# Performance work log

Measured on AMD Instinct MI355X. Metric: run time of the kernel, lower is better.

Reference implementation:

```python
import jax, jax.numpy as jnp
import numpy as np

N_NODES = 100000
N_EDGES = 1600000
D = 128


def setup_inputs() -> dict:
    key = jax.random.key(0)
    ks = jax.random.split(key, 10)
    s = 1.0 / np.sqrt(D)
    return {
        "feat": jax.random.normal(ks[0], (N_NODES, D), dtype=jnp.float32),
        "W_self0": jax.random.normal(ks[1], (D, D), dtype=jnp.float32) * s,
        "W_neigh0": jax.random.normal(ks[2], (D, D), dtype=jnp.float32) * s,
        "b0": jnp.zeros((D,), dtype=jnp.float32),
        "W_self1": jax.random.normal(ks[3], (D, D), dtype=jnp.float32) * s,
        "W_neigh1": jax.random.normal(ks[4], (D, D), dtype=jnp.float32) * s,
        "b1": jnp.zeros((D,), dtype=jnp.float32),
        "ln_g": jnp.ones((D,), dtype=jnp.float32),
        "ln_b": jnp.zeros((D,), dtype=jnp.float32),
        "edge_src": jax.random.randint(ks[5], (N_EDGES,), 0, N_NODES, dtype=jnp.int32),
        "edge_dst": jax.random.randint(ks[6], (N_EDGES,), 0, N_NODES, dtype=jnp.int32),
        "in_deg": jax.random.randint(ks[7], (N_NODES,), 1, 64, dtype=jnp.int32),
    }


def _sage_layer(h, src, dst, inv_deg, W_self, W_neigh, b):
    # mean aggregation over incoming neighbors: gather -> segment_sum -> scale
    msg = jax.ops.segment_sum(h[src], dst, num_segments=N_NODES)  # [N, d]
    h_neigh = msg * inv_deg[:, None]
    return h @ W_self + h_neigh @ W_neigh + b


def _layer_norm(x, g, b, eps=1e-5):
    mu = jnp.mean(x, axis=-1, keepdims=True)
    var = jnp.mean((x - mu) ** 2, axis=-1, keepdims=True)
    return (x - mu) * jax.lax.rsqrt(var + eps) * g + b


def reference(feat, W_self0, W_neigh0, b0, W_self1, W_neigh1, b1, ln_g, ln_b,
              edge_src, edge_dst, in_deg):
    # Eval mode: dropout = identity, no EmbeddingSelector / reg loss.
    inv_deg = 1.0 / jnp.maximum(in_deg, 1).astype(feat.dtype)
    h = _sage_layer(feat, edge_src, edge_dst, inv_deg, W_self0, W_neigh0, b0)
    h = _layer_norm(h, ln_g, ln_b)
    h = jax.nn.relu(h)
    h = _sage_layer(h, edge_src, edge_dst, inv_deg, W_self1, W_neigh1, b1)
    return h
```

## Files before the change

### kernel.cpp

```cpp
#include <hip/hip_runtime.h>

#define D 128
#define NN 100000

typedef __attribute__((ext_vector_type(8))) short short8;
typedef __attribute__((ext_vector_type(16))) float floatx16;
typedef __attribute__((ext_vector_type(2))) float floatx2;

__device__ inline unsigned short bf16_rne(float f) {
    unsigned int u = __float_as_uint(f);
    u += 0x7fff + ((u >> 16) & 1);
    return (unsigned short)(u >> 16);
}
__device__ inline unsigned char fp8_enc1(float f) {
    return (unsigned char)(__builtin_amdgcn_cvt_pk_fp8_f32(f, f, 0, false) & 0xff);
}

__global__ __launch_bounds__(256) void prep_kernel(
    const float* __restrict__ feat, unsigned short* __restrict__ feat16,
    unsigned char* __restrict__ feat8,
    const float* __restrict__ Ws0, const float* __restrict__ Wn0,
    const float* __restrict__ Ws1, const float* __restrict__ Wn1,
    unsigned short* __restrict__ wt0, unsigned short* __restrict__ wt1,
    int* __restrict__ counts)
{
    int bid = blockIdx.x;
    if (bid < 12500) {
        int i = bid * 256 + threadIdx.x;
        float4 v = *(const float4*)(feat + (size_t)i * 4);
        unsigned short u[4] = { bf16_rne(v.x), bf16_rne(v.y), bf16_rne(v.z), bf16_rne(v.w) };
        *(uint2*)(feat16 + (size_t)i * 4) = *(uint2*)u;
        int w = __builtin_amdgcn_cvt_pk_fp8_f32(v.x, v.y, 0, false);
        w = __builtin_amdgcn_cvt_pk_fp8_f32(v.z, v.w, w, true);
        ((unsigned int*)feat8)[i] = (unsigned int)w;
    } else if (bid < 12756) {
        int i = (bid - 12500) * 256 + threadIdx.x;
        int layer = i >> 15;
        int r = i & 32767;
        int n = r >> 8;
        int k = r & 255;
        const float* Ws = layer ? Ws1 : Ws0;
        const float* Wn = layer ? Wn1 : Wn0;
        float v = (k < 128) ? Ws[(size_t)k * 128 + n] : Wn[(size_t)(k - 128) * 128 + n];
        unsigned short* wt = layer ? wt1 : wt0;
        wt[(size_t)n * 256 + k] = bf16_rne(v);
    } else {
        int i = (bid - 12756) * 256 + threadIdx.x;
        if (i < NN / 4) ((uint4*)counts)[i] = make_uint4(0u, 0u, 0u, 0u);
    }
}

__global__ __launch_bounds__(256) void hist_rank_kernel(
    const int* __restrict__ dst, int* __restrict__ counts,
    int* __restrict__ rank, int E)
{
    int e = blockIdx.x * 256 + threadIdx.x;
    if (e < E) rank[e] = atomicAdd(&counts[dst[e]], 1);
}

__global__ __launch_bounds__(256) void scan1_kernel(
    const int* __restrict__ counts, int* __restrict__ row_ptr,
    int* __restrict__ blockSums, int N)
{
    __shared__ int sd[256];
    int t = threadIdx.x;
    int base = blockIdx.x * 1024;
    int v[4]; int tot = 0;
#pragma unroll
    for (int i = 0; i < 4; i++) {
        int idx = base + t * 4 + i;
        v[i] = (idx < N) ? counts[idx] : 0;
        tot += v[i];
    }
    sd[t] = tot; __syncthreads();
    for (int off = 1; off < 256; off <<= 1) {
        int x = (t >= off) ? sd[t - off] : 0;
        __syncthreads();
        sd[t] += x;
        __syncthreads();
    }
    int excl = sd[t] - tot;
    if (t == 255) blockSums[blockIdx.x] = sd[255];
    int run = excl;
#pragma unroll
    for (int i = 0; i < 4; i++) {
        int idx = base + t * 4 + i;
        if (idx < N) row_ptr[idx] = run;
        run += v[i];
    }
}

__global__ __launch_bounds__(256) void scan2_kernel(
    const int* __restrict__ blockSums, int* __restrict__ blockOffs, int nb)
{
    __shared__ int sd[256];
    int t = threadIdx.x;
    int val = (t < nb) ? blockSums[t] : 0;
    sd[t] = val; __syncthreads();
    for (int off = 1; off < 256; off <<= 1) {
        int x = (t >= off) ? sd[t - off] : 0;
        __syncthreads();
        sd[t] += x;
        __syncthreads();
    }
    if (t < nb) blockOffs[t] = sd[t] - val;
}

__global__ __launch_bounds__(256) void scan3_kernel(
    int* __restrict__ row_ptr, const int* __restrict__ blockOffs, int N, int E)
{
    int i = blockIdx.x * 256 + threadIdx.x;
    if (i < N) row_ptr[i] += blockOffs[i >> 10];
    if (i == N) row_ptr[N] = E;
}

__global__ __launch_bounds__(256) void fill_stream_kernel(
    const int* __restrict__ src, const int* __restrict__ dst,
    const int* __restrict__ row_ptr, const int* __restrict__ rank,
    int* __restrict__ col, int E)
{
    int e = blockIdx.x * 256 + threadIdx.x;
    if (e >= E) return;
    col[row_ptr[dst[e]] + rank[e]] = src[e];
}

__global__ __launch_bounds__(256) void gather8_kernel(
    const unsigned char* __restrict__ h8, const int* __restrict__ row_ptr,
    const int* __restrict__ col, const int* __restrict__ in_deg,
    unsigned short* __restrict__ msg16, int N)
{
    const int wave = threadIdx.x >> 6;
    const int lane = threadIdx.x & 63;
    const int quad = lane >> 4;
    const int ln16 = lane & 15;
    const int node = (blockIdx.x * 4 + wave) * 4 + quad;
    if (node >= N) return;

    const size_t lo = (size_t)ln16 * 8;
    int beg = row_ptr[node];
    int end = row_ptr[node + 1];

    float f[8] = {0.f,0.f,0.f,0.f,0.f,0.f,0.f,0.f};
    int j = beg;
    for (; j + 4 <= end; j += 4) {
        int c0 = col[j], c1 = col[j + 1], c2 = col[j + 2], c3 = col[j + 3];
        uint2 u0 = *(const uint2*)(h8 + (size_t)c0 * D + lo);
        uint2 u1 = *(const uint2*)(h8 + (size_t)c1 * D + lo);
        uint2 u2 = *(const uint2*)(h8 + (size_t)c2 * D + lo);
        uint2 u3 = *(const uint2*)(h8 + (size_t)c3 * D + lo);
#pragma unroll
        for (int q = 0; q < 4; q++) {
            uint2 u = q == 0 ? u0 : q == 1 ? u1 : q == 2 ? u2 : u3;
            floatx2 p0 = __builtin_amdgcn_cvt_pk_f32_fp8((int)u.x, false);
            floatx2 p1 = __builtin_amdgcn_cvt_pk_f32_fp8((int)u.x, true);
            floatx2 p2 = __builtin_amdgcn_cvt_pk_f32_fp8((int)u.y, false);
            floatx2 p3 = __builtin_amdgcn_cvt_pk_f32_fp8((int)u.y, true);
            f[0] += p0.x; f[1] += p0.y; f[2] += p1.x; f[3] += p1.y;
            f[4] += p2.x; f[5] += p2.y; f[6] += p3.x; f[7] += p3.y;
        }
    }
    for (; j < end; ++j) {
        uint2 u = *(const uint2*)(h8 + (size_t)col[j] * D + lo);
        floatx2 p0 = __builtin_amdgcn_cvt_pk_f32_fp8((int)u.x, false);
        floatx2 p1 = __builtin_amdgcn_cvt_pk_f32_fp8((int)u.x, true);
        floatx2 p2 = __builtin_amdgcn_cvt_pk_f32_fp8((int)u.y, false);
        floatx2 p3 = __builtin_amdgcn_cvt_pk_f32_fp8((int)u.y, true);
        f[0] += p0.x; f[1] += p0.y; f[2] += p1.x; f[3] += p1.y;
        f[4] += p2.x; f[5] += p2.y; f[6] += p3.x; f[7] += p3.y;
    }
    int dg = in_deg[node];
    float invd = 1.f / (float)(dg > 1 ? dg : 1);
    unsigned short us[8];
#pragma unroll
    for (int i = 0; i < 8; i++) us[i] = bf16_rne(f[i] * invd);
    *(uint4*)(msg16 + (size_t)node * D + ln16 * 8) = *(const uint4*)us;
}

__global__ __launch_bounds__(256) void mfma32_kernel(
    const unsigned short* __restrict__ A16, const unsigned short* __restrict__ Msg16,
    const unsigned short* __restrict__ Wt,
    const float* __restrict__ bias,
    const float* __restrict__ ln_g, const float* __restrict__ ln_b,
    unsigned short* __restrict__ Out16, unsigned char* __restrict__ Out8,
    float* __restrict__ Out32, int N, int do_ln)
{
    __shared__ unsigned short sB[32768];

    const int tid  = threadIdx.x;
    const int wave = tid >> 6;
    const int lane = tid & 63;
    const int half = lane >> 5;
    const int n32  = lane & 31;
    const int wrow0 = blockIdx.x * 128 + wave * 32;

#pragma unroll
    for (int i = 0; i < 16; i++) {
        int idx = tid + i * 256;
        int n = idx & 127;
        int c = idx >> 7;
        uint4 w = *(const uint4*)(Wt + (size_t)n * 256 + c * 8);
        int hs = c >> 4, kc = (c >> 1) & 7, hf = c & 1;
        int ct = n >> 5, nn = n & 31;
        int chunk = (((ct * 2 + hs) * 8 + kc) * 2 + hf) * 32 + nn;
        *(uint4*)&sB[(size_t)chunk * 8] = w;
    }
    __syncthreads();

    const int arow = wrow0 + n32;
    const bool arv = arow < N;
    const size_t koff = (size_t)half * 8;

    floatx16 acc[4];
#pragma unroll
    for (int ct = 0; ct < 4; ct++)
#pragma unroll
        for (int r = 0; r < 16; r++) acc[ct][r] = 0.f;

#pragma unroll
    for (int hs = 0; hs < 2; hs++) {
        const unsigned short* Asrc = hs ? Msg16 : A16;
#pragma unroll
        for (int kc = 0; kc < 8; kc++) {
            short8 a;
            if (arv) a = *(const short8*)(Asrc + (size_t)arow * D + kc * 16 + koff);
            else     a = (short8){0,0,0,0,0,0,0,0};
#pragma unroll
            for (int ct = 0; ct < 4; ct++) {
                short8 b = *(const short8*)&sB[((size_t)((ct * 2 + hs) * 8 + kc) * 64 + lane) * 8];
                acc[ct] = __builtin_amdgcn_mfma_f32_32x32x16_bf16(a, b, acc[ct], 0, 0, 0);
            }
        }
    }

    float bb[4];
#pragma unroll
    for (int ct = 0; ct < 4; ct++) bb[ct] = bias[ct * 32 + n32];

    float v[4][16];
#pragma unroll
    for (int ct = 0; ct < 4; ct++)
#pragma unroll
        for (int r = 0; r < 16; r++) v[ct][r] = acc[ct][r] + bb[ct];

    if (do_ln) {
        float gg[4], be[4];
#pragma unroll
        for (int ct = 0; ct < 4; ct++) {
            gg[ct] = ln_g[ct * 32 + n32];
            be[ct] = ln_b[ct * 32 + n32];
        }
        float s[16], s2[16];
#pragma unroll
        for (int r = 0; r < 16; r++) {
            s[r]  = v[0][r] + v[1][r] + v[2][r] + v[3][r];
            s2[r] = v[0][r]*v[0][r] + v[1][r]*v[1][r] + v[2][r]*v[2][r] + v[3][r]*v[3][r];
        }
#pragma unroll
        for (int off = 1; off < 32; off <<= 1) {
#pragma unroll
            for (int r = 0; r < 16; r++) {
                s[r]  += __shfl_xor(s[r],  off);
                s2[r] += __shfl_xor(s2[r], off);
            }
        }
#pragma unroll
        for (int r = 0; r < 16; r++) {
            float mean = s[r] * (1.f / 128.f);
            float var  = s2[r] * (1.f / 128.f) - mean * mean;
            float rstd = rsqrtf(var + 1e-5f);
            int row_g = wrow0 + (r & 3) + 8 * (r >> 2) + 4 * half;
            if (row_g < N) {
#pragma unroll
                for (int ct = 0; ct < 4; ct++) {
                    float t = (v[ct][r] - mean) * rstd * gg[ct] + be[ct];
                    t = t > 0.f ? t : 0.f;
                    Out16[(size_t)row_g * D + ct * 32 + n32] = bf16_rne(t);
                    Out8[(size_t)row_g * D + ct * 32 + n32] = fp8_enc1(t);
                }
            }
        }
    } else {
#pragma unroll
        for (int r = 0; r < 16; r++) {
            int row_g = wrow0 + (r & 3) + 8 * (r >> 2) + 4 * half;
            if (row_g < N) {
#pragma unroll
                for (int ct = 0; ct < 4; ct++)
                    Out32[(size_t)row_g * D + ct * 32 + n32] = v[ct][r];
            }
        }
    }
}

extern "C" void kernel_launch(void* const* d_in, const int* in_sizes, int n_in,
                              void* d_out, int out_size, void* d_ws, size_t ws_size,
                              hipStream_t stream)
{
    const float* feat = (const float*)d_in[0];
    const float* Ws0  = (const float*)d_in[1];
    const float* Wn0  = (const float*)d_in[2];
    const float* b0   = (const float*)d_in[3];
    const float* Ws1  = (const float*)d_in[4];
    const float* Wn1  = (const float*)d_in[5];
    const float* b1   = (const float*)d_in[6];
    const float* lng  = (const float*)d_in[7];
    const float* lnb  = (const float*)d_in[8];
    const int* esrc   = (const int*)d_in[9];
    const int* edst   = (const int*)d_in[10];
    const int* indeg  = (const int*)d_in[11];

    const int N = NN;
    const int E = in_sizes[9];

    float* out = (float*)d_out;

    char* ws = (char*)d_ws;
    size_t o = 0;
    auto alloc = [&](size_t bytes) { char* p = ws + o; o += (bytes + 15) & ~(size_t)15; return p; };
    unsigned short* feat16 = (unsigned short*)alloc((size_t)N * D * 2);
    int* col     = (int*)alloc((size_t)E * 4);
    int* row_ptr = (int*)alloc((size_t)(N + 1) * 4);
    unsigned short* wt0 = (unsigned short*)alloc(128 * 256 * 2);
    unsigned short* wt1 = (unsigned short*)alloc(128 * 256 * 2);
    int* bsums = (int*)alloc(1024);
    int* boffs = (int*)alloc(1024);
    char* regD = alloc((size_t)N * D * 2 > ((size_t)N * 4 + (size_t)E * 4 + 32)
                       ? (size_t)N * D * 2 : ((size_t)N * 4 + (size_t)E * 4 + 32));
    int* counts = (int*)regD;
    int* rank   = (int*)(regD + (((size_t)N * 4 + 15) & ~(size_t)15));
    unsigned short* h116 = (unsigned short*)regD;

    unsigned short* msg0 = (unsigned short*)d_out;
    unsigned char*  feat8 = (unsigned char*)d_out + (size_t)N * D * 2;
    unsigned char*  h18   = (unsigned char*)d_out + (size_t)N * D * 3;
    unsigned short* msg1 = feat16;
    (void)ws_size;

    const int edge_blocks = (E + 255) / 256;
    const int gemm_blocks = (N + 127) / 128;
    const int gather_blocks = (N + 15) / 16;
    const int nb = (N + 1023) / 1024;
    const int zero_blocks = (N / 4 + 255) / 256;

    prep_kernel<<<12500 + 256 + zero_blocks, 256, 0, stream>>>(
        feat, feat16, feat8, Ws0, Wn0, Ws1, Wn1, wt0, wt1, counts);

    hist_rank_kernel<<<edge_blocks, 256, 0, stream>>>(edst, counts, rank, E);
    scan1_kernel<<<nb, 256, 0, stream>>>(counts, row_ptr, bsums, N);
    scan2_kernel<<<1, 256, 0, stream>>>(bsums, boffs, nb);
    scan3_kernel<<<(N + 256) / 256, 256, 0, stream>>>(row_ptr, boffs, N, E);
    fill_stream_kernel<<<edge_blocks, 256, 0, stream>>>(esrc, edst, row_ptr, rank, col, E);

    gather8_kernel<<<gather_blocks, 256, 0, stream>>>(feat8, row_ptr, col, indeg, msg0, N);
    mfma32_kernel<<<gemm_blocks, 256, 0, stream>>>(
        feat16, msg0, wt0, b0, lng, lnb, h116, h18, nullptr, N, 1);

    gather8_kernel<<<gather_blocks, 256, 0, stream>>>(h18, row_ptr, col, indeg, msg1, N);
    mfma32_kernel<<<gemm_blocks, 256, 0, stream>>>(
        h116, msg1, wt1, b1, nullptr, nullptr, nullptr, nullptr, out, N, 0);
}
```

Measured before the change: 371.8 us.

## Build CSR via two-level bucket partition instead of global atomic histogram

Replaces the global-atomic histogram, three-kernel scan and random scatter with a two-pass radix-style partition. Edges are first bucketed by dst>>8 using LDS histograms and packed src/low-dst pairs, then each bucket is sorted locally in LDS to produce row_ptr and col. The aim is to cut global atomic contention and scattered writes, giving more localized memory traffic. In exchange it adds a packed intermediate array and assumes src fits in 24 bits and N fits within 391*256 buckets.

```diff
diff --git a/kernel.cpp b/kernel.cpp
--- a/kernel.cpp
+++ b/kernel.cpp
@@ -2,6 +2,8 @@
 
 #define D 128
 #define NN 100000
+#define PB 391
+#define EPB 4096
 
 typedef __attribute__((ext_vector_type(8))) short short8;
 typedef __attribute__((ext_vector_type(16))) float floatx16;
@@ -21,8 +23,7 @@
     unsigned char* __restrict__ feat8,
     const float* __restrict__ Ws0, const float* __restrict__ Wn0,
     const float* __restrict__ Ws1, const float* __restrict__ Wn1,
-    unsigned short* __restrict__ wt0, unsigned short* __restrict__ wt1,
-    int* __restrict__ counts)
+    unsigned short* __restrict__ wt0, unsigned short* __restrict__ wt1)
 {
     int bid = blockIdx.x;
     if (bid < 12500) {
@@ -33,7 +34,7 @@
         int w = __builtin_amdgcn_cvt_pk_fp8_f32(v.x, v.y, 0, false);
         w = __builtin_amdgcn_cvt_pk_fp8_f32(v.z, v.w, w, true);
         ((unsigned int*)feat8)[i] = (unsigned int)w;
-    } else if (bid < 12756) {
+    } else {
         int i = (bid - 12500) * 256 + threadIdx.x;
         int layer = i >> 15;
         int r = i & 32767;
@@ -44,84 +45,108 @@
         float v = (k < 128) ? Ws[(size_t)k * 128 + n] : Wn[(size_t)(k - 128) * 128 + n];
         unsigned short* wt = layer ? wt1 : wt0;
         wt[(size_t)n * 256 + k] = bf16_rne(v);
-    } else {
-        int i = (bid - 12756) * 256 + threadIdx.x;
-        if (i < NN / 4) ((uint4*)counts)[i] = make_uint4(0u, 0u, 0u, 0u);
-    }
-}
-
-__global__ __launch_bounds__(256) void hist_rank_kernel(
-    const int* __restrict__ dst, int* __restrict__ counts,
-    int* __restrict__ rank, int E)
-{
-    int e = blockIdx.x * 256 + threadIdx.x;
-    if (e < E) rank[e] = atomicAdd(&counts[dst[e]], 1);
-}
-
-__global__ __launch_bounds__(256) void scan1_kernel(
-    const int* __restrict__ counts, int* __restrict__ row_ptr,
-    int* __restrict__ blockSums, int N)
-{
-    __shared__ int sd[256];
+    }
+}
+
+__global__ __launch_bounds__(256) void part_count_kernel(
+    const int* __restrict__ dst, unsigned int* __restrict__ bucketCnt,
+    unsigned int* __restrict__ blockBase, int E)
+{
+    __shared__ unsigned int h[PB];
+    const int t = threadIdx.x;
+    const int b = blockIdx.x;
+    for (int i = t; i < PB; i += 256) h[i] = 0;
+    __syncthreads();
+    const int base = b * EPB;
+#pragma unroll
+    for (int k = 0; k < EPB / 256; k++) {
+        int e = base + k * 256 + t;
+        if (e < E) atomicAdd(&h[(unsigned)dst[e] >> 8], 1u);
+    }
+    __syncthreads();
+    for (int i = t; i < PB; i += 256) {
+        unsigned int c = h[i];
+        unsigned int o = 0;
+        if (c) o = atomicAdd(&bucketCnt[i], c);
+        blockBase[(size_t)b * PB + i] = o;
+    }
+}
+
+__global__ __launch_bounds__(512) void part_scan_kernel(
+    const unsigned int* __restrict__ bucketCnt, unsigned int* __restrict__ bucketStart,
+    int E)
+{
+    __shared__ unsigned int sd[512];
     int t = threadIdx.x;
-    int base = blockIdx.x * 1024;
-    int v[4]; int tot = 0;
-#pragma unroll
-    for (int i = 0; i < 4; i++) {
-        int idx = base + t * 4 + i;
-        v[i] = (idx < N) ? counts[idx] : 0;
-        tot += v[i];
-    }
-    sd[t] = tot; __syncthreads();
-    for (int off = 1; off < 256; off <<= 1) {
-        int x = (t >= off) ? sd[t - off] : 0;
+    unsigned int v = (t < PB) ? bucketCnt[t] : 0u;
+    sd[t] = v; __syncthreads();
+    for (int off = 1; off < 512; off <<= 1) {
+        unsigned int x = (t >= off) ? sd[t - off] : 0u;
         __syncthreads();
         sd[t] += x;
         __syncthreads();
     }
-    int excl = sd[t] - tot;
-    if (t == 255) blockSums[blockIdx.x] = sd[255];
-    int run = excl;
-#pragma unroll
-    for (int i = 0; i < 4; i++) {
-        int idx = base + t * 4 + i;
-        if (idx < N) row_ptr[idx] = run;
-        run += v[i];
-    }
-}
-
-__global__ __launch_bounds__(256) void scan2_kernel(
-    const int* __restrict__ blockSums, int* __restrict__ blockOffs, int nb)
-{
-    __shared__ int sd[256];
-    int t = threadIdx.x;
-    int val = (t < nb) ? blockSums[t] : 0;
-    sd[t] = val; __syncthreads();
+    if (t < PB) bucketStart[t] = sd[t] - v;
+    if (t == 0) bucketStart[PB] = (unsigned int)E;
+}
+
+__global__ __launch_bounds__(256) void part_scatter_kernel(
+    const int* __restrict__ src, const int* __restrict__ dst,
+    const unsigned int* __restrict__ bucketStart,
+    const unsigned int* __restrict__ blockBase,
+    unsigned int* __restrict__ pairs, int E)
+{
+    __shared__ unsigned int h[PB];
+    const int t = threadIdx.x;
+    const int b = blockIdx.x;
+    for (int i = t; i < PB; i += 256) h[i] = 0;
+    __syncthreads();
+    const int base = b * EPB;
+#pragma unroll
+    for (int k = 0; k < EPB / 256; k++) {
+        int e = base + k * 256 + t;
+        if (e < E) {
+            unsigned int d = (unsigned int)dst[e];
+            unsigned int bk = d >> 8;
+            unsigned int lr = atomicAdd(&h[bk], 1u);
+            unsigned int pos = bucketStart[bk] + blockBase[(size_t)b * PB + bk] + lr;
+            pairs[pos] = ((unsigned int)src[e] << 8) | (d & 255u);
+        }
+    }
+}
+
+__global__ __launch_bounds__(256) void part_fine_kernel(
+    const unsigned int* __restrict__ pairs, const unsigned int* __restrict__ bucketStart,
+    int* __restrict__ row_ptr, int* __restrict__ col, int N, int E)
+{
+    __shared__ unsigned int h[256], sc[256], pos[256];
+    const int t = threadIdx.x;
+    const int b = blockIdx.x;
+    h[t] = 0;
+    __syncthreads();
+    const unsigned int ebeg = bucketStart[b];
+    const unsigned int eend = bucketStart[b + 1];
+    for (unsigned int i = ebeg + t; i < eend; i += 256)
+        atomicAdd(&h[pairs[i] & 255u], 1u);
+    __syncthreads();
+    sc[t] = h[t]; __syncthreads();
     for (int off = 1; off < 256; off <<= 1) {
-        int x = (t >= off) ? sd[t - off] : 0;
+        unsigned int x = (t >= off) ? sc[t - off] : 0u;
         __syncthreads();
-        sd[t] += x;
+        sc[t] += x;
         __syncthreads();
     }
-    if (t < nb) blockOffs[t] = sd[t] - val;
-}
-
-__global__ __launch_bounds__(256) void scan3_kernel(
-    int* __restrict__ row_ptr, const int* __restrict__ blockOffs, int N, int E)
-{
-    int i = blockIdx.x * 256 + threadIdx.x;
-    if (i < N) row_ptr[i] += blockOffs[i >> 10];
-    if (i == N) row_ptr[N] = E;
-}
-
-__global__ __launch_bounds__(256) void fill_stream_kernel(
-    const int* __restrict__ src, const int* __restrict__ dst,
-    const int* __restrict__ row_ptr, const int* __restrict__ rank,
-    int* __restrict__ col, int E)
-{
-    int e = blockIdx.x * 256 + threadIdx.x;
-    if (e >= E) return;
-    col[row_ptr[dst[e]] + rank[e]] = src[e];
+    unsigned int excl = sc[t] - h[t];
+    int node = b * 256 + t;
+    if (node < N) row_ptr[node] = (int)(ebeg + excl);
+    pos[t] = ebeg + excl;
+    if (b == 0 && t == 0) row_ptr[N] = E;
+    __syncthreads();
+    for (unsigned int i = ebeg + t; i < eend; i += 256) {
+        unsigned int p = pairs[i];
+        unsigned int w = atomicAdd(&pos[p & 255u], 1u);
+        col[w] = (int)(p >> 8);
+    }
 }
 
 __global__ __launch_bounds__(256) void gather8_kernel(
@@ -314,6 +339,7 @@
 
     float* out = (float*)d_out;
 
+    const int nblk = (E + EPB - 1) / EPB;
     char* ws = (char*)d_ws;
     size_t o = 0;
     auto alloc = [&](size_t bytes) { char* p = ws + o; o += (bytes + 15) & ~(size_t)15; return p; };
@@ -322,34 +348,31 @@
     int* row_ptr = (int*)alloc((size_t)(N + 1) * 4);
     unsigned short* wt0 = (unsigned short*)alloc(128 * 256 * 2);
     unsigned short* wt1 = (unsigned short*)alloc(128 * 256 * 2);
-    int* bsums = (int*)alloc(1024);
-    int* boffs = (int*)alloc(1024);
-    char* regD = alloc((size_t)N * D * 2 > ((size_t)N * 4 + (size_t)E * 4 + 32)
-                       ? (size_t)N * D * 2 : ((size_t)N * 4 + (size_t)E * 4 + 32));
-    int* counts = (int*)regD;
-    int* rank   = (int*)(regD + (((size_t)N * 4 + 15) & ~(size_t)15));
+    size_t csr_bytes = (size_t)(512 + 512 + (size_t)nblk * PB + E) * 4 + 64;
+    char* regD = alloc((size_t)N * D * 2 > csr_bytes ? (size_t)N * D * 2 : csr_bytes);
+    unsigned int* bucketCnt   = (unsigned int*)regD;
+    unsigned int* bucketStart = bucketCnt + 512;
+    unsigned int* blockBase   = bucketStart + 512;
+    unsigned int* pairs       = blockBase + (size_t)nblk * PB;
     unsigned short* h116 = (unsigned short*)regD;
 
-    unsigned short* msg0 = (unsigned short*)d_out;
+    unsigned short* msg0  = (unsigned short*)d_out;
     unsigned char*  feat8 = (unsigned char*)d_out + (size_t)N * D * 2;
     unsigned char*  h18   = (unsigned char*)d_out + (size_t)N * D * 3;
-    unsigned short* msg1 = feat16;
+    unsigned short* msg1  = feat16;
     (void)ws_size;
 
-    const int edge_blocks = (E + 255) / 256;
     const int gemm_blocks = (N + 127) / 128;
     const int gather_blocks = (N + 15) / 16;
-    const int nb = (N + 1023) / 1024;
-    const int zero_blocks = (N / 4 + 255) / 256;
-
-    prep_kernel<<<12500 + 256 + zero_blocks, 256, 0, stream>>>(
-        feat, feat16, feat8, Ws0, Wn0, Ws1, Wn1, wt0, wt1, counts);
-
-    hist_rank_kernel<<<edge_blocks, 256, 0, stream>>>(edst, counts, rank, E);
-    scan1_kernel<<<nb, 256, 0, stream>>>(counts, row_ptr, bsums, N);
-    scan2_kernel<<<1, 256, 0, stream>>>(bsums, boffs, nb);
-    scan3_kernel<<<(N + 256) / 256, 256, 0, stream>>>(row_ptr, boffs, N, E);
-    fill_stream_kernel<<<edge_blocks, 256, 0, stream>>>(esrc, edst, row_ptr, rank, col, E);
+
+    prep_kernel<<<12500 + 256, 256, 0, stream>>>(
+        feat, feat16, feat8, Ws0, Wn0, Ws1, Wn1, wt0, wt1);
+
+    hipMemsetAsync(bucketCnt, 0, 512 * 4, stream);
+    part_count_kernel<<<nblk, 256, 0, stream>>>(edst, bucketCnt, blockBase, E);
+    part_scan_kernel<<<1, 512, 0, stream>>>(bucketCnt, bucketStart, E);
+    part_scatter_kernel<<<nblk, 256, 0, stream>>>(esrc, edst, bucketStart, blockBase, pairs, E);
+    part_fine_kernel<<<PB, 256, 0, stream>>>(pairs, bucketStart, row_ptr, col, N, E);
 
     gather8_kernel<<<gather_blocks, 256, 0, stream>>>(feat8, row_ptr, col, indeg, msg0, N);
     mfma32_kernel<<<gemm_blocks, 256, 0, stream>>>(
```

After: 319.7 us. -14.0%, faster.
